# Kernel tuning notes

Measured on AMD Instinct MI355X. Metric: run time of the kernel, lower is better.

## Reference

```python
import jax, jax.numpy as jnp
import numpy as np

NUM_NET = 2
V = 100000
D = 128
B = 4096
K = 5
NS = 10
HYP1 = 0.1
HYP2 = 0.1
HYP3 = 0.1


def setup_inputs() -> dict:
    key = jax.random.key(0)
    ks = jax.random.split(key, 10)
    ri = lambda k, shape: jax.random.randint(k, shape, 0, V, dtype=jnp.int32)
    return {
        "node_tables": jax.random.normal(ks[0], (NUM_NET, V, D), jnp.float32) * 0.1,
        "neigh_tables": jax.random.normal(ks[1], (NUM_NET, V, D), jnp.float32) * 0.1,
        "nodes_idx": ri(ks[2], (NUM_NET, B)),
        "neigh_idx": ri(ks[3], (NUM_NET, B, K)),
        "role_idx": ri(ks[4], (NUM_NET, NUM_NET, B)),
        "neg_main": ri(ks[5], (NUM_NET, B, K * NS)),
        "neg_node": ri(ks[6], (NUM_NET, NUM_NET, B, 1 * NS)),
        "neg_cross": ri(ks[7], (NUM_NET, NUM_NET, B, K * NS)),
        "neg_role": ri(ks[8], (NUM_NET, NUM_NET, B, 1 * NS)),
    }


def _pos_loss(ctx, node):
    # ctx: (B, M, D), node: (B, D) -> mean over all logsigmoid(ctx . node)
    return jax.nn.log_sigmoid(jnp.einsum("bmd,bd->bm", ctx, node)).mean()


def _neg_loss(neg_ctx, node):
    # ctx embeddings are negated: logsigmoid(-(neg . node)), sum over samples, mean over batch
    return jax.nn.log_sigmoid(-jnp.einsum("bmd,bd->bm", neg_ctx, node)).sum(axis=1).mean()


def reference(node_tables, neigh_tables, nodes_idx, neigh_idx, role_idx,
              neg_main, neg_node, neg_cross, neg_role):
    cost = []
    for i in range(NUM_NET):
        node_emb = node_tables[i][nodes_idx[i]]          # (B, D)
        # main SGNS loss on view i (neigh tables)
        neigh_emb = neigh_tables[i][neigh_idx[i]]        # (B, K, D)
        c = _pos_loss(neigh_emb, node_emb) + _neg_loss(neigh_tables[i][neg_main[i]], node_emb)
        cost.append(c)
        # cross-view node alignment (node tables of j at same node indices)
        for j in range(NUM_NET):
            if j != i:
                ctx = node_tables[j][nodes_idx[i]][:, None, :]   # (B, 1, D)
                c = _pos_loss(ctx, node_emb) + _neg_loss(node_tables[j][neg_node[i, j]], node_emb)
                cost.append(HYP1 * c)
        # cross-view neighbor loss (neigh tables of j at view-i neighbor indices)
        for j in range(NUM_NET):
            if j != i:
                ctx = neigh_tables[j][neigh_idx[i]]              # (B, K, D)
                c = _pos_loss(ctx, node_emb) + _neg_loss(neigh_tables[j][neg_cross[i, j]], node_emb)
                cost.append(HYP2 * c)
        # role-based loss (node tables of all j at role indices)
        for j in range(NUM_NET):
            ctx = node_tables[j][role_idx[i, j]][:, None, :]     # (B, 1, D)
            c = _pos_loss(ctx, node_emb) + _neg_loss(node_tables[j][neg_role[i, j]], node_emb)
            cost.append(HYP3 * c)
    total = cost[0]
    for c in cost[1:]:
        total = total + c
    return -total / len(cost)
```

## Files before the change

### kernel.cpp

```cpp
#include <hip/hip_runtime.h>

#define NUM_NET 2
#define V 100000
#define D 128
#define B 4096
#define K 5
#define NS 10

#define W_MAIN_POS (1.0f/20480.0f)
#define W_INV_B    (1.0f/4096.0f)
#define HYP_B      (0.1f/4096.0f)
#define HYP2_BK    (0.1f/20480.0f)

#define NBINS 64

__global__ __launch_bounds__(256) void rmne_main(
    const float* __restrict__ node_tables,
    const float* __restrict__ neigh_tables,
    const int*   __restrict__ nodes_idx,
    const int*   __restrict__ neigh_idx,
    const int*   __restrict__ role_idx,
    const int*   __restrict__ neg_main,
    const int*   __restrict__ neg_node,
    const int*   __restrict__ neg_cross,
    const int*   __restrict__ neg_role,
    float*       __restrict__ ws)
{
    const int tid  = threadIdx.x;
    const int lane = tid & 63;
    const int wave = tid >> 6;
    const int unit = blockIdx.x * 4 + wave;
    const int i = unit >> 12;
    const int b = unit & (B - 1);
    const int j = 1 - i;

    int   pk[3];
    float wv[3];
    #pragma unroll
    for (int s = 0; s < 3; ++s) {
        int d = lane + 64 * s;
        int idx = 0; float w = 0.0f; int tab = 0;
        if      (d <   5) { idx = neigh_idx[(i*B + b)*K + d];              w =  W_MAIN_POS; tab = 2 + i; }
        else if (d <  55) { idx = neg_main[(i*B + b)*50 + (d-5)];          w = -W_INV_B;    tab = 2 + i; }
        else if (d <  56) { idx = nodes_idx[i*B + b];                      w =  HYP_B;      tab = j;     }
        else if (d <  66) { idx = neg_node[((i*2+j)*B + b)*NS + (d-56)];   w = -HYP_B;      tab = j;     }
        else if (d <  71) { idx = neigh_idx[(i*B + b)*K + (d-66)];         w =  HYP2_BK;    tab = 2 + j; }
        else if (d < 121) { idx = neg_cross[((i*2+j)*B + b)*50 + (d-71)];  w = -HYP_B;      tab = 2 + j; }
        else if (d < 122) { idx = role_idx[(i*2+0)*B + b];                 w =  HYP_B;      tab = 0;     }
        else if (d < 132) { idx = neg_role[((i*2+0)*B + b)*NS + (d-122)];  w = -HYP_B;      tab = 0;     }
        else if (d < 133) { idx = role_idx[(i*2+1)*B + b];                 w =  HYP_B;      tab = 1;     }
        else if (d < 143) { idx = neg_role[((i*2+1)*B + b)*NS + (d-133)];  w = -HYP_B;      tab = 1;     }
        pk[s] = idx | (tab << 20);
        wv[s] = w;
    }

    const int l16     = lane & 15;
    const int quarter = lane >> 4;
    const int nrow    = nodes_idx[i*B + b];
    const float4* nep = (const float4*)(node_tables + ((size_t)i*V + (size_t)nrow)*D) + l16*2;
    const float4 ne0 = nep[0];
    const float4 ne1 = nep[1];

    float acc = 0.0f;

    auto do_iter = [&](int t, int pks, float wvs) {
        int   src = (4*t + quarter) & 63;
        int   p   = __shfl(pks, src, 64);
        float w   = __shfl(wvs, src, 64);
        int idx = p & 0xFFFFF;
        int tab = p >> 20;
        const float* base = (tab & 2) ? neigh_tables : node_tables;
        const float4* row = (const float4*)(base + ((size_t)(tab & 1)*V + (size_t)idx)*D) + l16*2;
        float4 c0 = row[0];
        float4 c1 = row[1];
        float pp = ne0.x*c0.x + ne0.y*c0.y + ne0.z*c0.z + ne0.w*c0.w
                 + ne1.x*c1.x + ne1.y*c1.y + ne1.z*c1.z + ne1.w*c1.w;
        pp += __shfl_xor(pp, 1, 64);
        pp += __shfl_xor(pp, 2, 64);
        pp += __shfl_xor(pp, 4, 64);
        pp += __shfl_xor(pp, 8, 64);
        float x  = (w < 0.0f) ? -pp : pp;
        float ls = fminf(x, 0.0f) - __logf(1.0f + __expf(-fabsf(x)));
        acc += fabsf(w) * ls;
    };

    #pragma unroll 4
    for (int t = 0;  t < 16; ++t) do_iter(t, pk[0], wv[0]);
    #pragma unroll 4
    for (int t = 16; t < 32; ++t) do_iter(t, pk[1], wv[1]);
    #pragma unroll
    for (int t = 32; t < 36; ++t) do_iter(t, pk[2], wv[2]);

    acc += __shfl_xor(acc, 16, 64);
    acc += __shfl_xor(acc, 32, 64);

    __shared__ float wsum[4];
    if (lane == 0) wsum[wave] = acc;
    __syncthreads();
    if (tid == 0) {
        float s = wsum[0] + wsum[1] + wsum[2] + wsum[3];
        atomicAdd(ws + (blockIdx.x & (NBINS - 1)), s);
    }
}

__global__ void rmne_finalize(const float* __restrict__ ws, float* __restrict__ out)
{
    float v = ws[threadIdx.x];
    v += __shfl_xor(v, 1, 64);
    v += __shfl_xor(v, 2, 64);
    v += __shfl_xor(v, 4, 64);
    v += __shfl_xor(v, 8, 64);
    v += __shfl_xor(v, 16, 64);
    v += __shfl_xor(v, 32, 64);
    if (threadIdx.x == 0) out[0] = v * (-1.0f / 10.0f);
}

extern "C" void kernel_launch(void* const* d_in, const int* in_sizes, int n_in,
                              void* d_out, int out_size, void* d_ws, size_t ws_size,
                              hipStream_t stream) {
    const float* node_tables  = (const float*)d_in[0];
    const float* neigh_tables = (const float*)d_in[1];
    const int*   nodes_idx    = (const int*)d_in[2];
    const int*   neigh_idx    = (const int*)d_in[3];
    const int*   role_idx     = (const int*)d_in[4];
    const int*   neg_main     = (const int*)d_in[5];
    const int*   neg_node     = (const int*)d_in[6];
    const int*   neg_cross    = (const int*)d_in[7];
    const int*   neg_role     = (const int*)d_in[8];
    float* ws  = (float*)d_ws;
    float* out = (float*)d_out;

    hipMemsetAsync(ws, 0, NBINS * sizeof(float), stream);
    rmne_main<<<2048, 256, 0, stream>>>(node_tables, neigh_tables, nodes_idx, neigh_idx,
                                        role_idx, neg_main, neg_node, neg_cross, neg_role, ws);
    rmne_finalize<<<1, 64, 0, stream>>>(ws, out);
}
```

Measured before the change: 263.4 us.

## Software-pipeline row gathers, use DPP reductions, and specialize weights per iteration

```diff
diff --git a/kernel.cpp b/kernel.cpp
--- a/kernel.cpp
+++ b/kernel.cpp
@@ -7,12 +7,23 @@
 #define K 5
 #define NS 10
 
-#define W_MAIN_POS (1.0f/20480.0f)
-#define W_INV_B    (1.0f/4096.0f)
-#define HYP_B      (0.1f/4096.0f)
-#define HYP2_BK    (0.1f/20480.0f)
+#define W_A (1.0f/20480.0f)
+#define W_B (1.0f/4096.0f)
+#define W_C (0.1f/4096.0f)
+#define W_D (0.1f/20480.0f)
 
 #define NBINS 64
+#define PIPE 4
+
+template <int CTRL>
+__device__ __forceinline__ float dpp_xadd(float v) {
+    int r = __builtin_amdgcn_update_dpp(0, __float_as_int(v), CTRL, 0xF, 0xF, true);
+    return v + __int_as_float(r);
+}
+
+__device__ __forceinline__ float lsig(float x) {
+    return fminf(x, 0.0f) - __logf(1.0f + __expf(-fabsf(x)));
+}
 
 __global__ __launch_bounds__(256) void rmne_main(
     const float* __restrict__ node_tables,
@@ -34,24 +45,22 @@
     const int b = unit & (B - 1);
     const int j = 1 - i;
 
-    int   pk[3];
-    float wv[3];
+    int pk[3];
     #pragma unroll
     for (int s = 0; s < 3; ++s) {
         int d = lane + 64 * s;
-        int idx = 0; float w = 0.0f; int tab = 0;
-        if      (d <   5) { idx = neigh_idx[(i*B + b)*K + d];              w =  W_MAIN_POS; tab = 2 + i; }
-        else if (d <  55) { idx = neg_main[(i*B + b)*50 + (d-5)];          w = -W_INV_B;    tab = 2 + i; }
-        else if (d <  56) { idx = nodes_idx[i*B + b];                      w =  HYP_B;      tab = j;     }
-        else if (d <  66) { idx = neg_node[((i*2+j)*B + b)*NS + (d-56)];   w = -HYP_B;      tab = j;     }
-        else if (d <  71) { idx = neigh_idx[(i*B + b)*K + (d-66)];         w =  HYP2_BK;    tab = 2 + j; }
-        else if (d < 121) { idx = neg_cross[((i*2+j)*B + b)*50 + (d-71)];  w = -HYP_B;      tab = 2 + j; }
-        else if (d < 122) { idx = role_idx[(i*2+0)*B + b];                 w =  HYP_B;      tab = 0;     }
-        else if (d < 132) { idx = neg_role[((i*2+0)*B + b)*NS + (d-122)];  w = -HYP_B;      tab = 0;     }
-        else if (d < 133) { idx = role_idx[(i*2+1)*B + b];                 w =  HYP_B;      tab = 1;     }
-        else if (d < 143) { idx = neg_role[((i*2+1)*B + b)*NS + (d-133)];  w = -HYP_B;      tab = 1;     }
+        int idx = 0; int tab = 0;
+        if      (d <   5) { idx = neigh_idx[(i*B + b)*K + d];             tab = 2 + i; }
+        else if (d <  55) { idx = neg_main[(i*B + b)*50 + (d-5)];         tab = 2 + i; }
+        else if (d <  56) { idx = nodes_idx[i*B + b];                     tab = j;     }
+        else if (d <  66) { idx = neg_node[((i*2+j)*B + b)*NS + (d-56)];  tab = j;     }
+        else if (d <  71) { idx = neigh_idx[(i*B + b)*K + (d-66)];        tab = 2 + j; }
+        else if (d < 121) { idx = neg_cross[((i*2+j)*B + b)*50 + (d-71)]; tab = 2 + j; }
+        else if (d < 122) { idx = role_idx[(i*2+0)*B + b];                tab = 0;     }
+        else if (d < 132) { idx = neg_role[((i*2+0)*B + b)*NS + (d-122)]; tab = 0;     }
+        else if (d < 133) { idx = role_idx[(i*2+1)*B + b];                tab = 1;     }
+        else if (d < 143) { idx = neg_role[((i*2+1)*B + b)*NS + (d-133)]; tab = 1;     }
         pk[s] = idx | (tab << 20);
-        wv[s] = w;
     }
 
     const int l16     = lane & 15;
@@ -61,35 +70,78 @@
     const float4 ne0 = nep[0];
     const float4 ne1 = nep[1];
 
-    float acc = 0.0f;
+    float4 c0b[PIPE], c1b[PIPE];
 
-    auto do_iter = [&](int t, int pks, float wvs) {
-        int   src = (4*t + quarter) & 63;
-        int   p   = __shfl(pks, src, 64);
-        float w   = __shfl(wvs, src, 64);
+    auto issue = [&](int t) {
+        int s   = t >> 4;
+        int src = (4*t + quarter) & 63;
+        int p   = __shfl(pk[s], src, 64);
         int idx = p & 0xFFFFF;
         int tab = p >> 20;
         const float* base = (tab & 2) ? neigh_tables : node_tables;
         const float4* row = (const float4*)(base + ((size_t)(tab & 1)*V + (size_t)idx)*D) + l16*2;
-        float4 c0 = row[0];
-        float4 c1 = row[1];
+        c0b[t & (PIPE-1)] = row[0];
+        c1b[t & (PIPE-1)] = row[1];
+    };
+
+    float accA = 0.0f, accB = 0.0f, accC = 0.0f, accG = 0.0f;
+
+    #pragma unroll
+    for (int t = 0; t < PIPE; ++t) issue(t);
+
+    #pragma unroll
+    for (int t = 0; t < 36; ++t) {
+        if (t + PIPE < 36) issue(t + PIPE);
+        float4 c0 = c0b[t & (PIPE-1)];
+        float4 c1 = c1b[t & (PIPE-1)];
         float pp = ne0.x*c0.x + ne0.y*c0.y + ne0.z*c0.z + ne0.w*c0.w
                  + ne1.x*c1.x + ne1.y*c1.y + ne1.z*c1.z + ne1.w*c1.w;
-        pp += __shfl_xor(pp, 1, 64);
-        pp += __shfl_xor(pp, 2, 64);
-        pp += __shfl_xor(pp, 4, 64);
-        pp += __shfl_xor(pp, 8, 64);
-        float x  = (w < 0.0f) ? -pp : pp;
-        float ls = fminf(x, 0.0f) - __logf(1.0f + __expf(-fabsf(x)));
-        acc += fabsf(w) * ls;
-    };
+        pp = dpp_xadd<0xB1>(pp);
+        pp = dpp_xadd<0x4E>(pp);
+        pp = dpp_xadd<0x124>(pp);
+        pp = dpp_xadd<0x128>(pp);
 
-    #pragma unroll 4
-    for (int t = 0;  t < 16; ++t) do_iter(t, pk[0], wv[0]);
-    #pragma unroll 4
-    for (int t = 16; t < 32; ++t) do_iter(t, pk[1], wv[1]);
-    #pragma unroll
-    for (int t = 32; t < 36; ++t) do_iter(t, pk[2], wv[2]);
+        if (t == 0) {
+            accA += lsig(pp);
+        } else if (t == 1) {
+            float x  = (quarter == 0) ? pp : -pp;
+            float mw = (quarter == 0) ? W_A : W_B;
+            accG = fmaf(mw, lsig(x), accG);
+        } else if (t <= 12) {
+            accB += lsig(-pp);
+        } else if (t == 13) {
+            float x  = (quarter == 3) ? pp : -pp;
+            float mw = (quarter == 3) ? W_C : W_B;
+            accG = fmaf(mw, lsig(x), accG);
+        } else if (t <= 15) {
+            accC += lsig(-pp);
+        } else if (t == 16) {
+            float x  = (quarter >= 2) ? pp : -pp;
+            float mw = (quarter >= 2) ? W_D : W_C;
+            accG = fmaf(mw, lsig(x), accG);
+        } else if (t == 17) {
+            float x  = (quarter == 3) ? -pp : pp;
+            float mw = (quarter == 3) ? W_C : W_D;
+            accG = fmaf(mw, lsig(x), accG);
+        } else if (t <= 29) {
+            accC += lsig(-pp);
+        } else if (t == 30) {
+            float x = (quarter == 1) ? pp : -pp;
+            accC += lsig(x);
+        } else if (t <= 32) {
+            accC += lsig(-pp);
+        } else if (t == 33) {
+            float x = (quarter == 0) ? pp : -pp;
+            accC += lsig(x);
+        } else if (t == 34) {
+            accC += lsig(-pp);
+        } else {
+            float ls = lsig(-pp);
+            accC += (quarter == 3) ? 0.0f : ls;
+        }
+    }
+
+    float acc = W_A*accA + W_B*accB + W_C*accC + accG;
 
     acc += __shfl_xor(acc, 16, 64);
     acc += __shfl_xor(acc, 32, 64);
```

New measurement: 255.4 us, median of 2. -3.0%, faster.
